# Performance work log

Measured on AMD Instinct MI355X. Metric: run time of the kernel, lower is better.

## Reference

```python
import jax, jax.numpy as jnp
import numpy as np

B, L, D = 32, 1024, 128

def setup_inputs() -> dict:
    key = jax.random.key(0)
    kq, kk, kv, ks = jax.random.split(key, 4)
    Q = jax.random.normal(kq, (B, L, D), dtype=jnp.float32)
    K = jax.random.normal(kk, (B, L, D), dtype=jnp.float32)
    V = jax.random.normal(kv, (B, L, D), dtype=jnp.float32)
    kg_sim = jax.random.uniform(ks, (B, L, L), dtype=jnp.float32)
    scale = jnp.float32(1.0 / np.sqrt(D))
    return {"Q": Q, "K": K, "V": V, "scale": scale, "kg_sim": kg_sim}

def reference(Q, K, V, scale, kg_sim):
    # attention = -1 * (Q @ K^T) * scale   [B, L, L]
    attn = -scale * jnp.einsum('bqd,bkd->bqk', Q, K)
    # attention = -softmax(attention, axis=-1)
    attn = -jax.nn.softmax(attn, axis=-1)
    # beta = softmax(attention * kg_sim, axis=-1)
    beta = jax.nn.softmax(attn * kg_sim, axis=-1)
    # context = beta @ V   [B, L, D]
    return jnp.einsum('bqk,bkd->bqd', beta, V)
```

## Files before the change

### kernel.cpp

```cpp
#include <hip/hip_runtime.h>
#include <hip/hip_bf16.h>

#define L 1024
#define D 128
#define NB 32
#define BQ 16

typedef __attribute__((ext_vector_type(8))) short short8;
typedef __attribute__((ext_vector_type(4))) short short4v;
typedef __attribute__((ext_vector_type(4))) float f32x4;

__device__ __forceinline__ unsigned short f2bf(float f) {
    union { float f; unsigned int u; } x; x.f = f;
    unsigned int r = x.u + 0x7FFF + ((x.u >> 16) & 1);
    return (unsigned short)(r >> 16);
}
__device__ __forceinline__ float bf2f(unsigned short u) {
    union { unsigned int u; float f; } x; x.u = ((unsigned int)u) << 16;
    return x.f;
}

__global__ void prep_kernel(const float* __restrict__ K, const float* __restrict__ V,
                            unsigned short* __restrict__ Kb, unsigned short* __restrict__ Vt) {
    __shared__ unsigned short t[32][40];
    int id = blockIdx.x;
    int tid = threadIdx.x;
    if (id < 2048) {
        size_t base = (size_t)id * 2048 + (size_t)tid * 8;
        float4 a = *(const float4*)(K + base);
        float4 c = *(const float4*)(K + base + 4);
        short8 o;
        o[0] = (short)f2bf(a.x); o[1] = (short)f2bf(a.y);
        o[2] = (short)f2bf(a.z); o[3] = (short)f2bf(a.w);
        o[4] = (short)f2bf(c.x); o[5] = (short)f2bf(c.y);
        o[6] = (short)f2bf(c.z); o[7] = (short)f2bf(c.w);
        *(short8*)(Kb + base) = o;
        return;
    }
    id -= 2048;
    int b = id >> 7;
    int rest = id & 127;
    int kt = rest >> 2, dt = rest & 3;
    int k0 = kt * 32, d0 = dt * 32;

    int kl = tid >> 3, dl4 = (tid & 7) * 4;
    const float* src = V + (((size_t)b * L + (k0 + kl)) * D) + d0 + dl4;
    float4 v = *(const float4*)src;
    t[dl4 + 0][kl] = f2bf(v.x);
    t[dl4 + 1][kl] = f2bf(v.y);
    t[dl4 + 2][kl] = f2bf(v.z);
    t[dl4 + 3][kl] = f2bf(v.w);
    __syncthreads();

    int dl = tid >> 3, kl4 = (tid & 7) * 4;
    unsigned short* dst = Vt + (((size_t)b * D + (d0 + dl)) * L) + k0 + kl4;
    short4v o;
    o[0] = (short)t[dl][kl4 + 0];
    o[1] = (short)t[dl][kl4 + 1];
    o[2] = (short)t[dl][kl4 + 2];
    o[3] = (short)t[dl][kl4 + 3];
    *(short4v*)dst = o;
}

__global__ __launch_bounds__(256, 4)
void attn_kernel(const float* __restrict__ Q, const unsigned short* __restrict__ Kb,
                 const float* __restrict__ scale_p, const float* __restrict__ kg,
                 const unsigned short* __restrict__ Vt, float* __restrict__ out) {
    __shared__ unsigned short S16[BQ * 1032];
    __shared__ float zpart[4][BQ];
    __shared__ float row_scale[BQ];

    const int tid = threadIdx.x;
    const int b  = blockIdx.x >> 6;
    const int q0 = (blockIdx.x & 63) * BQ;
    const float nsc = -scale_p[0];

    const int wave = tid >> 6, lane = tid & 63;
    const int lr = lane & 15;
    const int lg = lane >> 4;
    const int row = tid >> 4, l = tid & 15;

    const float* kgrow = kg + (((size_t)b * L) + q0 + row) * L + l * 4;
    float4 kgv[16];
#pragma unroll
    for (int j = 0; j < 16; j++) kgv[j] = *(const float4*)(kgrow + 64 * j);
    __builtin_amdgcn_sched_barrier(0);

    short8 aq[4];
#pragma unroll
    for (int kb = 0; kb < 4; kb++) {
        const float* qp = Q + (((size_t)b * L) + q0 + lr) * D + kb * 32 + lg * 8;
        float4 v0 = *(const float4*)qp;
        float4 v1 = *(const float4*)(qp + 4);
        short8 o;
        o[0] = (short)f2bf(v0.x * nsc); o[1] = (short)f2bf(v0.y * nsc);
        o[2] = (short)f2bf(v0.z * nsc); o[3] = (short)f2bf(v0.w * nsc);
        o[4] = (short)f2bf(v1.x * nsc); o[5] = (short)f2bf(v1.y * nsc);
        o[6] = (short)f2bf(v1.z * nsc); o[7] = (short)f2bf(v1.w * nsc);
        aq[kb] = o;
    }

    f32x4 zp = {0.f, 0.f, 0.f, 0.f};
#pragma unroll 2
    for (int i = 0; i < 16; i++) {
        int ct = wave + i * 4;
        const unsigned short* kp = Kb + (((size_t)b * L) + ct * 16 + lr) * D + lg * 8;
        f32x4 acc = {0.f, 0.f, 0.f, 0.f};
#pragma unroll
        for (int kb = 0; kb < 4; kb++) {
            short8 bf = *(const short8*)(kp + kb * 32);
            acc = __builtin_amdgcn_mfma_f32_16x16x32_bf16(aq[kb], bf, acc, 0, 0, 0);
        }
#pragma unroll
        for (int r = 0; r < 4; r++) {
            float p = __expf(acc[r]);
            S16[(lg * 4 + r) * 1032 + ct * 16 + lr] = f2bf(p);
            zp[r] += p;
        }
    }
#pragma unroll
    for (int m = 1; m < 16; m <<= 1) {
#pragma unroll
        for (int r = 0; r < 4; r++) zp[r] += __shfl_xor(zp[r], m, 64);
    }
    if (lr == 0) {
#pragma unroll
        for (int r = 0; r < 4; r++) zpart[wave][lg * 4 + r] = zp[r];
    }
    __syncthreads();

    const float iz1 = 1.0f / (zpart[0][row] + zpart[1][row] +
                              zpart[2][row] + zpart[3][row]);
    unsigned short* srow = &S16[row * 1032];
    float z2 = 0.f;
#pragma unroll
    for (int j = 0; j < 16; j++) {
        unsigned short* p = &srow[l * 4 + 64 * j];
        short4v v = *(const short4v*)p;
        float4 g = kgv[j];
        float e0 = __expf(-(bf2f((unsigned short)v[0]) * iz1) * g.x);
        float e1 = __expf(-(bf2f((unsigned short)v[1]) * iz1) * g.y);
        float e2 = __expf(-(bf2f((unsigned short)v[2]) * iz1) * g.z);
        float e3 = __expf(-(bf2f((unsigned short)v[3]) * iz1) * g.w);
        z2 += (e0 + e1) + (e2 + e3);
        short4v o; o[0] = (short)f2bf(e0); o[1] = (short)f2bf(e1);
        o[2] = (short)f2bf(e2); o[3] = (short)f2bf(e3);
        *(short4v*)p = o;
    }
#pragma unroll
    for (int m = 1; m < 16; m <<= 1) z2 += __shfl_xor(z2, m, 64);
    if (l == 0) row_scale[row] = 1.0f / z2;
    __syncthreads();

    const int dt0 = wave * 2;
    f32x4 acc0 = {0.f, 0.f, 0.f, 0.f}, acc1 = {0.f, 0.f, 0.f, 0.f};
    const unsigned short* vt0 = Vt + (((size_t)b * D) + dt0 * 16 + lr) * L + lg * 8;
    const unsigned short* vt1 = vt0 + (size_t)16 * L;
    const unsigned short* brow = &S16[lr * 1032 + lg * 8];
#pragma unroll 8
    for (int kb = 0; kb < 32; kb++) {
        short8 a  = *(const short8*)(brow + kb * 32);
        short8 b0 = *(const short8*)(vt0 + kb * 32);
        short8 b1 = *(const short8*)(vt1 + kb * 32);
        acc0 = __builtin_amdgcn_mfma_f32_16x16x32_bf16(a, b0, acc0, 0, 0, 0);
        acc1 = __builtin_amdgcn_mfma_f32_16x16x32_bf16(a, b1, acc1, 0, 0, 0);
    }
    float* orow = out + (((size_t)b * L) + q0) * D;
#pragma unroll
    for (int r = 0; r < 4; r++) {
        int rq = lg * 4 + r;
        float rs = row_scale[rq];
        orow[(size_t)rq * D + dt0 * 16 + lr]       = acc0[r] * rs;
        orow[(size_t)rq * D + (dt0 + 1) * 16 + lr] = acc1[r] * rs;
    }
}

extern "C" void kernel_launch(void* const* d_in, const int* in_sizes, int n_in,
                              void* d_out, int out_size, void* d_ws, size_t ws_size,
                              hipStream_t stream) {
    const float* Q     = (const float*)d_in[0];
    const float* K     = (const float*)d_in[1];
    const float* V     = (const float*)d_in[2];
    const float* scale = (const float*)d_in[3];
    const float* kg    = (const float*)d_in[4];
    float* out = (float*)d_out;
    unsigned short* Vt = (unsigned short*)d_ws;
    unsigned short* Kb = (unsigned short*)d_ws + (size_t)NB * D * L;

    prep_kernel<<<6144, 256, 0, stream>>>(K, V, Kb, Vt);
    attn_kernel<<<NB * (L / BQ), 256, 0, stream>>>(Q, Kb, scale, kg, Vt, out);
}
```

Measured before the change: 341.7 us.

## Keep first-softmax exponentials in registers and fuse second softmax per lane

Swaps the MFMA operand order so each lane holds exponentials for a single query row across key columns. Those values stay packed as bf16 in registers, so the first pass no longer writes them to shared memory and reads them back. kg_sim is now loaded with nontemporal loads in two halves after the QK pass rather than prefetched upfront, and the second softmax is computed directly from registers. The aim is to cut LDS traffic and register pressure from the 16 float4 prefetch, at the cost of a 32-register packed buffer and kg load latency that now falls inside the critical path.

```diff
diff --git a/kernel.cpp b/kernel.cpp
--- a/kernel.cpp
+++ b/kernel.cpp
@@ -67,8 +67,8 @@
                  const float* __restrict__ scale_p, const float* __restrict__ kg,
                  const unsigned short* __restrict__ Vt, float* __restrict__ out) {
     __shared__ unsigned short S16[BQ * 1032];
-    __shared__ float zpart[4][BQ];
-    __shared__ float row_scale[BQ];
+    __shared__ float zp1[4][BQ];
+    __shared__ float zp2[4][BQ];
 
     const int tid = threadIdx.x;
     const int b  = blockIdx.x >> 6;
@@ -78,13 +78,6 @@
     const int wave = tid >> 6, lane = tid & 63;
     const int lr = lane & 15;
     const int lg = lane >> 4;
-    const int row = tid >> 4, l = tid & 15;
-
-    const float* kgrow = kg + (((size_t)b * L) + q0 + row) * L + l * 4;
-    float4 kgv[16];
-#pragma unroll
-    for (int j = 0; j < 16; j++) kgv[j] = *(const float4*)(kgrow + 64 * j);
-    __builtin_amdgcn_sched_barrier(0);
 
     short8 aq[4];
 #pragma unroll
@@ -100,56 +93,80 @@
         aq[kb] = o;
     }
 
-    f32x4 zp = {0.f, 0.f, 0.f, 0.f};
-#pragma unroll 2
+    unsigned int pP[32];
+    float z1p = 0.f;
+#pragma unroll
     for (int i = 0; i < 16; i++) {
         int ct = wave + i * 4;
         const unsigned short* kp = Kb + (((size_t)b * L) + ct * 16 + lr) * D + lg * 8;
         f32x4 acc = {0.f, 0.f, 0.f, 0.f};
 #pragma unroll
         for (int kb = 0; kb < 4; kb++) {
-            short8 bf = *(const short8*)(kp + kb * 32);
-            acc = __builtin_amdgcn_mfma_f32_16x16x32_bf16(aq[kb], bf, acc, 0, 0, 0);
+            short8 kf = *(const short8*)(kp + kb * 32);
+            acc = __builtin_amdgcn_mfma_f32_16x16x32_bf16(kf, aq[kb], acc, 0, 0, 0);
         }
-#pragma unroll
-        for (int r = 0; r < 4; r++) {
-            float p = __expf(acc[r]);
-            S16[(lg * 4 + r) * 1032 + ct * 16 + lr] = f2bf(p);
-            zp[r] += p;
-        }
-    }
-#pragma unroll
-    for (int m = 1; m < 16; m <<= 1) {
-#pragma unroll
-        for (int r = 0; r < 4; r++) zp[r] += __shfl_xor(zp[r], m, 64);
-    }
-    if (lr == 0) {
-#pragma unroll
-        for (int r = 0; r < 4; r++) zpart[wave][lg * 4 + r] = zp[r];
-    }
+        float p0 = __expf(acc[0]);
+        float p1 = __expf(acc[1]);
+        float p2 = __expf(acc[2]);
+        float p3 = __expf(acc[3]);
+        z1p += (p0 + p1) + (p2 + p3);
+        pP[i * 2]     = ((unsigned int)f2bf(p1) << 16) | f2bf(p0);
+        pP[i * 2 + 1] = ((unsigned int)f2bf(p3) << 16) | f2bf(p2);
+    }
+    z1p += __shfl_xor(z1p, 16, 64);
+    z1p += __shfl_xor(z1p, 32, 64);
+    if (lg == 0) zp1[wave][lr] = z1p;
+
+    const float* kgq = kg + (((size_t)b * L) + q0 + lr) * L + wave * 16 + lg * 4;
+    f32x4 g0[8];
+#pragma unroll
+    for (int j = 0; j < 8; j++)
+        g0[j] = __builtin_nontemporal_load((const f32x4*)(kgq + 64 * j));
+
     __syncthreads();
 
-    const float iz1 = 1.0f / (zpart[0][row] + zpart[1][row] +
-                              zpart[2][row] + zpart[3][row]);
-    unsigned short* srow = &S16[row * 1032];
-    float z2 = 0.f;
-#pragma unroll
-    for (int j = 0; j < 16; j++) {
-        unsigned short* p = &srow[l * 4 + 64 * j];
-        short4v v = *(const short4v*)p;
-        float4 g = kgv[j];
-        float e0 = __expf(-(bf2f((unsigned short)v[0]) * iz1) * g.x);
-        float e1 = __expf(-(bf2f((unsigned short)v[1]) * iz1) * g.y);
-        float e2 = __expf(-(bf2f((unsigned short)v[2]) * iz1) * g.z);
-        float e3 = __expf(-(bf2f((unsigned short)v[3]) * iz1) * g.w);
-        z2 += (e0 + e1) + (e2 + e3);
+    const float iz1 = 1.0f / (zp1[0][lr] + zp1[1][lr] + zp1[2][lr] + zp1[3][lr]);
+    float z2p = 0.f;
+#pragma unroll
+    for (int j = 0; j < 8; j++) {
+        int ct = wave + j * 4;
+        float p0 = bf2f((unsigned short)(pP[j * 2] & 0xFFFF)) * iz1;
+        float p1 = bf2f((unsigned short)(pP[j * 2] >> 16)) * iz1;
+        float p2 = bf2f((unsigned short)(pP[j * 2 + 1] & 0xFFFF)) * iz1;
+        float p3 = bf2f((unsigned short)(pP[j * 2 + 1] >> 16)) * iz1;
+        float e0 = __expf(-p0 * g0[j][0]);
+        float e1 = __expf(-p1 * g0[j][1]);
+        float e2 = __expf(-p2 * g0[j][2]);
+        float e3 = __expf(-p3 * g0[j][3]);
+        z2p += (e0 + e1) + (e2 + e3);
         short4v o; o[0] = (short)f2bf(e0); o[1] = (short)f2bf(e1);
         o[2] = (short)f2bf(e2); o[3] = (short)f2bf(e3);
-        *(short4v*)p = o;
-    }
-#pragma unroll
-    for (int m = 1; m < 16; m <<= 1) z2 += __shfl_xor(z2, m, 64);
-    if (l == 0) row_scale[row] = 1.0f / z2;
+        *(short4v*)&S16[lr * 1032 + ct * 16 + lg * 4] = o;
+    }
+    f32x4 g1[8];
+#pragma unroll
+    for (int j = 0; j < 8; j++)
+        g1[j] = __builtin_nontemporal_load((const f32x4*)(kgq + 64 * (j + 8)));
+#pragma unroll
+    for (int j = 8; j < 16; j++) {
+        int ct = wave + j * 4;
+        f32x4 g = g1[j - 8];
+        float p0 = bf2f((unsigned short)(pP[j * 2] & 0xFFFF)) * iz1;
+        float p1 = bf2f((unsigned short)(pP[j * 2] >> 16)) * iz1;
+        float p2 = bf2f((unsigned short)(pP[j * 2 + 1] & 0xFFFF)) * iz1;
+        float p3 = bf2f((unsigned short)(pP[j * 2 + 1] >> 16)) * iz1;
+        float e0 = __expf(-p0 * g[0]);
+        float e1 = __expf(-p1 * g[1]);
+        float e2 = __expf(-p2 * g[2]);
+        float e3 = __expf(-p3 * g[3]);
+        z2p += (e0 + e1) + (e2 + e3);
+        short4v o; o[0] = (short)f2bf(e0); o[1] = (short)f2bf(e1);
+        o[2] = (short)f2bf(e2); o[3] = (short)f2bf(e3);
+        *(short4v*)&S16[lr * 1032 + ct * 16 + lg * 4] = o;
+    }
+    z2p += __shfl_xor(z2p, 16, 64);
+    z2p += __shfl_xor(z2p, 32, 64);
+    if (lg == 0) zp2[wave][lr] = z2p;
     __syncthreads();
 
     const int dt0 = wave * 2;
@@ -169,7 +186,7 @@
 #pragma unroll
     for (int r = 0; r < 4; r++) {
         int rq = lg * 4 + r;
-        float rs = row_scale[rq];
+        float rs = 1.0f / (zp2[0][rq] + zp2[1][rq] + zp2[2][rq] + zp2[3][rq]);
         orow[(size_t)rq * D + dt0 * 16 + lr]       = acc0[r] * rs;
         orow[(size_t)rq * D + (dt0 + 1) * 16 + lr] = acc1[r] * rs;
     }
```

Result: no change. 346.6 us (+1.4%).
